# Performance work log

Hardware: AMD Instinct MI355X
Metric: run time of the kernel (lower is better)

Reference implementation:

```python
import jax, jax.numpy as jnp
import numpy as np

HID = 3584   # hidden_size
NH = 28      # num_attention_heads
NKV = 4      # num_key_value_heads
HD = 128     # head_dim
S = 4        # packed samples
L = 1024     # tokens per sample (sample_lens = [L]*S)
T = S * L
THETA = 1000000.0
EPS = 1e-6


def rmsnorm(x, w):
    # Qwen2NavitRMSNorm (fp32 math)
    v = jnp.mean(x * x, axis=-1, keepdims=True)
    return w * (x * jax.lax.rsqrt(v + EPS))


def rotate_half(x):
    d = x.shape[-1] // 2
    return jnp.concatenate([-x[..., d:], x[..., :d]], axis=-1)


def setup_inputs() -> dict:
    key = jax.random.key(0)
    ks = jax.random.split(key, 12)
    sc = 0.02
    x = jax.random.normal(ks[0], (T, HID), jnp.float32)
    # rotary embeddings: positions restart per packed sample
    pos = jnp.tile(jnp.arange(L, dtype=jnp.float32), S)
    inv = 1.0 / (THETA ** (jnp.arange(0, HD, 2, dtype=jnp.float32) / HD))
    fr = pos[:, None] * inv[None, :]
    emb = jnp.concatenate([fr, fr], axis=-1)  # [T, HD]
    und_idx = jnp.arange(0, T, 2, dtype=jnp.int32)  # interleaved und/gen tokens
    gen_idx = jnp.arange(1, T, 2, dtype=jnp.int32)
    n = lambda k, shp: jax.random.normal(k, shp, jnp.float32) * sc
    return dict(
        packed_sequence=x, cos=jnp.cos(emb), sin=jnp.sin(emb),
        wq=n(ks[1], (NH * HD, HID)), bq=jnp.zeros((NH * HD,), jnp.float32),
        wk=n(ks[2], (NKV * HD, HID)), bk=jnp.zeros((NKV * HD,), jnp.float32),
        wv=n(ks[3], (NKV * HD, HID)), bv=jnp.zeros((NKV * HD,), jnp.float32),
        wo=n(ks[4], (HID, NH * HD)),
        wqg=n(ks[5], (NH * HD, HID)), bqg=jnp.zeros((NH * HD,), jnp.float32),
        wkg=n(ks[6], (NKV * HD, HID)), bkg=jnp.zeros((NKV * HD,), jnp.float32),
        wvg=n(ks[7], (NKV * HD, HID)), bvg=jnp.zeros((NKV * HD,), jnp.float32),
        wog=n(ks[8], (HID, NH * HD)),
        qn=jnp.ones((HD,), jnp.float32), kn=jnp.ones((HD,), jnp.float32),
        qng=jnp.ones((HD,), jnp.float32), kng=jnp.ones((HD,), jnp.float32),
        und_idx=und_idx, gen_idx=gen_idx,
    )


def reference(packed_sequence, cos, sin, wq, bq, wk, bk, wv, bv, wo,
              wqg, bqg, wkg, bkg, wvg, bvg, wog, qn, kn, qng, kng,
              und_idx, gen_idx):
    x = packed_sequence
    xu = x[und_idx]
    xg = x[gen_idx]

    def dual_proj(wu, bu, wg, bg, dim):
        out = jnp.zeros((T, dim), x.dtype)
        out = out.at[und_idx].set(xu @ wu.T + bu)
        out = out.at[gen_idx].set(xg @ wg.T + bg)
        return out

    q = dual_proj(wq, bq, wqg, bqg, NH * HD).reshape(T, NH, HD)
    k = dual_proj(wk, bk, wkg, bkg, NKV * HD).reshape(T, NKV, HD)
    v = dual_proj(wv, bv, wvg, bvg, NKV * HD).reshape(T, NKV, HD)

    # per-modality qk RMSNorm
    q = jnp.zeros_like(q).at[und_idx].set(rmsnorm(q[und_idx], qn)).at[gen_idx].set(rmsnorm(q[gen_idx], qng))
    k = jnp.zeros_like(k).at[und_idx].set(rmsnorm(k[und_idx], kn)).at[gen_idx].set(rmsnorm(k[gen_idx], kng))

    # RoPE (unsqueeze_dim=1 -> broadcast over heads)
    c = cos[:, None, :]
    s = sin[:, None, :]
    q = q * c + rotate_half(q) * s
    k = k * c + rotate_half(k) * s

    # GQA expand kv heads (consecutive repeat matches repeat+reshape in torch)
    grp = NH // NKV
    k = jnp.repeat(k, grp, axis=1)  # [T, NH, HD]
    v = jnp.repeat(v, grp, axis=1)

    # packed -> per-sample causal attention (all sample_lens equal)
    qh = q.reshape(S, L, NH, HD)
    kh = k.reshape(S, L, NH, HD)
    vh = v.reshape(S, L, NH, HD)
    scores = jnp.einsum('slhd,smhd->shlm', qh, kh) / np.float32(np.sqrt(HD))
    causal = jnp.tril(jnp.ones((L, L), bool))
    scores = jnp.where(causal, scores, jnp.float32(-1e30))
    p = jax.nn.softmax(scores, axis=-1)
    attn = jnp.einsum('shlm,smhd->slhd', p, vh).reshape(T, NH * HD)

    out = jnp.zeros((T, HID), x.dtype)
    out = out.at[und_idx].set(attn[und_idx] @ wo.T)
    out = out.at[gen_idx].set(attn[gen_idx] @ wog.T)
    return out
```

## Files before the change

### kernel.cpp

```cpp
#include <hip/hip_runtime.h>
#include <hip/hip_bf16.h>

#define T_TOK 4096
#define HID   3584
#define NH    28
#define NKV   4
#define HD    128
#define SEG   4
#define LSEQ  1024
#define KDIM  3584
#define BKG   64
#define NCVT  128

typedef __attribute__((ext_vector_type(8))) short bf16x8;
typedef __attribute__((ext_vector_type(4))) float f32x4;

#define GLOAD16(g, l) __builtin_amdgcn_global_load_lds( \
    (const __attribute__((address_space(1))) void*)(g), \
    (__attribute__((address_space(3))) void*)(l), 16, 0, 0)

__device__ __forceinline__ unsigned short f2bf(float f) {
    unsigned u = __float_as_uint(f);
    return (unsigned short)((u + 0x7fffu + ((u >> 16) & 1u)) >> 16);
}
__device__ __forceinline__ float bf2f(unsigned short u) {
    return __uint_as_float(((unsigned)u) << 16);
}

__device__ __forceinline__ f32x4 mfma16(bf16x8 a, bf16x8 b, f32x4 c) {
    return __builtin_amdgcn_mfma_f32_16x16x32_bf16(a, b, c, 0, 0, 0);
}

#define XN4  3670016
#define WQ4  3211264
#define WK4  458752
__global__ void cvt_front(const float* __restrict__ x,
                          const float* __restrict__ wq, const float* __restrict__ wqg,
                          const float* __restrict__ wk, const float* __restrict__ wkg,
                          const float* __restrict__ wv, const float* __restrict__ wvg,
                          unsigned short* __restrict__ xu, unsigned short* __restrict__ xg,
                          unsigned short* __restrict__ wqb, unsigned short* __restrict__ wqgb,
                          unsigned short* __restrict__ wkb, unsigned short* __restrict__ wkgb,
                          unsigned short* __restrict__ wvb, unsigned short* __restrict__ wvgb) {
    size_t i = (size_t)blockIdx.x * 256 + threadIdx.x;
    if (i < XN4) {
        int t = (int)(i / (HID / 4));
        int c = (int)(i - (size_t)t * (HID / 4));
        float4 v = reinterpret_cast<const float4*>(x)[i];
        ushort4 o;
        o.x = f2bf(v.x); o.y = f2bf(v.y); o.z = f2bf(v.z); o.w = f2bf(v.w);
        unsigned short* dst = ((t & 1) ? xg : xu) + (size_t)(t >> 1) * HID + c * 4;
        *reinterpret_cast<ushort4*>(dst) = o;
        return;
    }
    i -= XN4;
    const float* s; unsigned short* d;
    if (i < 2 * (size_t)WQ4) {
        if (i < WQ4) { s = wq; d = wqb; } else { i -= WQ4; s = wqg; d = wqgb; }
    } else {
        i -= 2 * (size_t)WQ4;
        size_t seg = i / WK4; i -= seg * WK4;
        switch (seg) {
            case 0: s = wk;  d = wkb;  break;
            case 1: s = wkg; d = wkgb; break;
            case 2: s = wv;  d = wvb;  break;
            default: s = wvg; d = wvgb; break;
        }
    }
    float4 v = reinterpret_cast<const float4*>(s)[i];
    ushort4 o;
    o.x = f2bf(v.x); o.y = f2bf(v.y); o.z = f2bf(v.z); o.w = f2bf(v.w);
    reinterpret_cast<ushort4*>(d)[i] = o;
}

__device__ __forceinline__ void gemm256_core(const unsigned short* __restrict__ Aptr,
                                             const unsigned short* __restrict__ Bptr,
                                             unsigned short* ldsbase, f32x4 (&acc)[8][4],
                                             int kb, int kend) {
    const int tid = threadIdx.x;
    const int lane = tid & 63, w = tid >> 6;
    const int wr = w >> 2, wc = w & 3;
    const int lr = lane & 15, lkg = lane >> 4;
    char* const L = (char*)ldsbase;

    int src_off[4];
#pragma unroll
    for (int j = 0; j < 4; j++) {
        int r = j * 64 + (tid >> 3);
        int clog = (tid & 7) ^ ((tid >> 3) & 7);
        src_off[j] = r * KDIM + clog * 8;
    }
    const int aoff0 = (wr * 128 + lr) * 128 + ((lkg ^ (lr & 7)) << 4);
    const int boff0 = (wc * 64 + lr) * 128 + ((lkg ^ (lr & 7)) << 4) + 32768;

    bf16x8 a[4][2], b[4][2];
#pragma unroll
    for (int m = 0; m < 8; m++)
#pragma unroll
        for (int n = 0; n < 4; n++) acc[m][n] = (f32x4){0.f, 0.f, 0.f, 0.f};

#define STG_A(buf, k0, h) do { _Pragma("unroll") for (int jj = 0; jj < 2; jj++) { \
    int j = (h) * 2 + jj; \
    GLOAD16(Aptr + src_off[j] + (k0), L + (buf) * 65536 + j * 8192 + tid * 16); } } while (0)
#define STG_B(buf, k0, h) do { _Pragma("unroll") for (int jj = 0; jj < 2; jj++) { \
    int j = (h) * 2 + jj; \
    GLOAD16(Bptr + src_off[j] + (k0), L + (buf) * 65536 + 32768 + j * 8192 + tid * 16); } } while (0)
#define RD_A(buf, mh) do { _Pragma("unroll") for (int mm = 0; mm < 4; mm++) { \
    int ro = (buf) * 65536 + aoff0 + ((mh) * 4 + mm) * 2048; \
    a[mm][0] = *(const bf16x8*)(L + ro); \
    a[mm][1] = *(const bf16x8*)(L + (ro ^ 64)); } } while (0)
#define RD_B(buf, nh) do { _Pragma("unroll") for (int nn = 0; nn < 2; nn++) { \
    int ro = (buf) * 65536 + boff0 + ((nh) * 2 + nn) * 2048; \
    b[(nh) * 2 + nn][0] = *(const bf16x8*)(L + ro); \
    b[(nh) * 2 + nn][1] = *(const bf16x8*)(L + (ro ^ 64)); } } while (0)
#define MM(mh, nh) do { _Pragma("unroll") for (int mm = 0; mm < 4; mm++) \
    _Pragma("unroll") for (int nn = 0; nn < 2; nn++) \
    _Pragma("unroll") for (int ks = 0; ks < 2; ks++) \
        acc[(mh) * 4 + mm][(nh) * 2 + nn] = \
            mfma16(a[mm][ks], b[(nh) * 2 + nn][ks], acc[(mh) * 4 + mm][(nh) * 2 + nn]); } while (0)
#define BAR   asm volatile("s_barrier" ::: "memory")
#define LGKM0 do { asm volatile("s_waitcnt lgkmcnt(0)" ::: "memory"); \
                   __builtin_amdgcn_sched_barrier(0); } while (0)
#define VMC4  asm volatile("s_waitcnt vmcnt(4)" ::: "memory")
#define PHI   __builtin_amdgcn_s_setprio(1)
#define PLO   __builtin_amdgcn_s_setprio(0)

    STG_A(0, kb, 0); STG_A(0, kb, 1); STG_B(0, kb, 0); STG_B(0, kb, 1);
    STG_B(1, kb + BKG, 0); STG_B(1, kb + BKG, 1);
    VMC4;
    BAR;

    const int iters = (kend - kb) / (2 * BKG);
#pragma unroll 1
    for (int t = 0; t < iters; ++t) {
        int k1 = kb + (2 * t + 1) * BKG;
        int k2 = kb + (2 * t + 2) * BKG; if (k2 > kend - BKG) k2 = kend - BKG;
        int k3 = kb + (2 * t + 3) * BKG; if (k3 > kend - BKG) k3 = kend - BKG;
        RD_A(0, 0); RD_B(0, 0); STG_A(1, k1, 0);
        BAR; LGKM0; PHI; MM(0, 0); PLO; BAR;
        RD_B(0, 1); STG_A(1, k1, 1);
        BAR; LGKM0; PHI; MM(0, 1); PLO; BAR;
        RD_A(0, 1); STG_B(0, k2, 0);
        BAR; LGKM0; PHI; MM(1, 0); PLO; BAR;
        STG_B(0, k2, 1);
        BAR; LGKM0; PHI; MM(1, 1); PLO; VMC4; BAR;
        RD_A(1, 0); RD_B(1, 0); STG_A(0, k2, 0);
        BAR; LGKM0; PHI; MM(0, 0); PLO; BAR;
        RD_B(1, 1); STG_A(0, k2, 1);
        BAR; LGKM0; PHI; MM(0, 1); PLO; BAR;
        RD_A(1, 1); STG_B(1, k3, 0);
        BAR; LGKM0; PHI; MM(1, 0); PLO; BAR;
        STG_B(1, k3, 1);
        BAR; LGKM0; PHI; MM(1, 1); PLO; VMC4; BAR;
    }
    asm volatile("s_waitcnt vmcnt(0)" ::: "memory");

#undef STG_A
#undef STG_B
#undef RD_A
#undef RD_B
#undef MM
#undef BAR
#undef LGKM0
#undef VMC4
#undef PHI
#undef PLO
}

__global__ __launch_bounds__(512, 2) void qkv_gemm8(
    const unsigned short* __restrict__ xu, const unsigned short* __restrict__ xg,
    const unsigned short* __restrict__ wq0, const unsigned short* __restrict__ wk0,
    const unsigned short* __restrict__ wv0, const unsigned short* __restrict__ wq1,
    const unsigned short* __restrict__ wk1, const unsigned short* __restrict__ wv1,
    const float* __restrict__ bq0, const float* __restrict__ bk0, const float* __restrict__ bv0,
    const float* __restrict__ bq1, const float* __restrict__ bk1, const float* __restrict__ bv1,
    unsigned short* __restrict__ qp, unsigned short* __restrict__ kp,
    unsigned short* __restrict__ vp) {
    __shared__ unsigned short lds[65536];
    const int bid = blockIdx.x;
    int nb, ks, bm, kb, klen;
    if (bid < 256) {
        int g = bid >> 6;
        int rem = bid & 63;
        ks = rem >> 4; bm = rem & 15;
        nb = 14 + g;
        kb = ks * 896; klen = 896;
    } else {
        int e = bid - 256;
        nb = e >> 4; bm = e & 15;
        ks = 0; kb = 0; klen = KDIM;
    }
    const int par = bm >> 3, mb = bm & 7;
    const unsigned short* A = (par ? xg : xu) + (size_t)mb * 256 * KDIM;
    const unsigned short* W;
    const float* bias;
    unsigned short* C;
    int ldc, col0;
    if (nb < 14) {
        W = (par ? wq1 : wq0) + (size_t)nb * 256 * KDIM;
        bias = (par ? bq1 : bq0); C = qp; ldc = NH * HD; col0 = nb * 256;
    } else if (nb < 16) {
        W = (par ? wk1 : wk0) + (size_t)(nb - 14) * 256 * KDIM;
        bias = (par ? bk1 : bk0); C = kp + (size_t)ks * T_TOK * (NKV * HD);
        ldc = NKV * HD; col0 = (nb - 14) * 256;
    } else {
        W = (par ? wv1 : wv0) + (size_t)(nb - 16) * 256 * KDIM;
        bias = (par ? bv1 : bv0); C = vp + (size_t)ks * T_TOK * (NKV * HD);
        ldc = NKV * HD; col0 = (nb - 16) * 256;
    }
    f32x4 acc[8][4];
    gemm256_core(A, W, lds, acc, kb, kb + klen);

    const int lane = threadIdx.x & 63, w = threadIdx.x >> 6;
    const int wr = w >> 2, wc = w & 3, lr = lane & 15, lkg = lane >> 4;
#pragma unroll
    for (int n = 0; n < 4; n++) {
        int colt = col0 + wc * 64 + n * 16 + lr;
        float bb = (ks == 0) ? bias[colt] : 0.f;
#pragma unroll
        for (int m = 0; m < 8; m++) {
#pragma unroll
            for (int rg = 0; rg < 4; rg++) {
                int tr = mb * 256 + wr * 128 + m * 16 + lkg * 4 + rg;
                int tok = 2 * tr + par;
                C[(size_t)tok * ldc + colt] = f2bf(acc[m][n][rg] + bb);
            }
        }
    }
}

__global__ __launch_bounds__(512, 2) void oproj_gemm8(
    const unsigned short* __restrict__ au, const unsigned short* __restrict__ ag,
    const unsigned short* __restrict__ wo0, const unsigned short* __restrict__ wo1,
    float* __restrict__ out) {
    __shared__ unsigned short lds[65536];
    const int bid = blockIdx.x;
    const int x = bid & 7, i = bid >> 3;
    const int nb = i >> 1, bm = x * 2 + (i & 1);
    const int par = bm >> 3, mb = bm & 7;
    const unsigned short* A = (par ? ag : au) + (size_t)mb * 256 * KDIM;
    const unsigned short* W = (par ? wo1 : wo0) + (size_t)nb * 256 * KDIM;
    f32x4 acc[8][4];
    gemm256_core(A, W, lds, acc, 0, KDIM);

    const int lane = threadIdx.x & 63, w = threadIdx.x >> 6;
    const int wr = w >> 2, wc = w & 3, lr = lane & 15, lkg = lane >> 4;
#pragma unroll
    for (int n = 0; n < 4; n++) {
        int col = nb * 256 + wc * 64 + n * 16 + lr;
#pragma unroll
        for (int m = 0; m < 8; m++) {
#pragma unroll
            for (int rg = 0; rg < 4; rg++) {
                int tr = mb * 256 + wr * 128 + m * 16 + lkg * 4 + rg;
                int tok = 2 * tr + par;
                out[(size_t)tok * HID + col] = acc[m][n][rg];
            }
        }
    }
}

__global__ void normrope2(const unsigned short* __restrict__ qp, const unsigned short* __restrict__ kp,
                          const unsigned short* __restrict__ vp,
                          const float* __restrict__ cosb, const float* __restrict__ sinb,
                          const float* __restrict__ qn, const float* __restrict__ kn,
                          const float* __restrict__ qng, const float* __restrict__ kng,
                          unsigned short* __restrict__ q_bf, unsigned short* __restrict__ k_bf,
                          unsigned short* __restrict__ vT) {
    if (blockIdx.y == 8) {
        if (blockIdx.x >= 1024) return;
        const int u = blockIdx.x * 2 + (threadIdx.x >> 7);
        const int d = threadIdx.x & 127;
        const int sh = u >> 7, lb = u & 127;
        const int s = sh >> 2, hv = sh & 3;
        const size_t S = (size_t)T_TOK * NKV * HD;
        unsigned short tmp[8];
#pragma unroll
        for (int i = 0; i < 8; i++) {
            size_t idx = ((size_t)(s * LSEQ + lb * 8 + i)) * (NKV * HD) + hv * HD + d;
            tmp[i] = f2bf(bf2f(vp[idx]) + bf2f(vp[S + idx]) +
                          bf2f(vp[2 * S + idx]) + bf2f(vp[3 * S + idx]));
        }
        *(bf16x8*)(vT + ((size_t)sh * HD + d) * LSEQ + lb * 8) = *(bf16x8*)tmp;
        return;
    }
    const int t = blockIdx.x, w = threadIdx.x >> 6, lane = threadIdx.x & 63;
    const int h = blockIdx.y * 4 + w;
    const bool isq = (h < 28);
    float v0, v1;
    if (isq) {
        const unsigned short* src = qp + (size_t)t * (NH * HD) + h * HD;
        v0 = bf2f(src[lane]);
        v1 = bf2f(src[lane + 64]);
    } else {
        const unsigned short* src = kp + (size_t)t * (NKV * HD) + (h - 28) * HD;
        const size_t S = (size_t)T_TOK * NKV * HD;
        v0 = bf2f(src[lane]) + bf2f(src[S + lane]) + bf2f(src[2 * S + lane]) + bf2f(src[3 * S + lane]);
        v1 = bf2f(src[lane + 64]) + bf2f(src[S + lane + 64]) +
             bf2f(src[2 * S + lane + 64]) + bf2f(src[3 * S + lane + 64]);
    }
    float ss = v0 * v0 + v1 * v1;
#pragma unroll
    for (int off = 32; off >= 1; off >>= 1) ss += __shfl_xor(ss, off, 64);
    float inv = rsqrtf(ss * (1.f / 128.f) + 1e-6f);
    const float* wn = isq ? ((t & 1) ? qng : qn) : ((t & 1) ? kng : kn);
    float n0 = v0 * inv * wn[lane], n1 = v1 * inv * wn[lane + 64];
    float c0 = cosb[(size_t)t * HD + lane], c1 = cosb[(size_t)t * HD + lane + 64];
    float s0 = sinb[(size_t)t * HD + lane], s1 = sinb[(size_t)t * HD + lane + 64];
    float o0 = n0 * c0 - n1 * s0;
    float o1 = n1 * c1 + n0 * s1;
    unsigned short* dst = isq ? q_bf + (size_t)t * (NH * HD) + h * HD
                              : k_bf + (size_t)t * (NKV * HD) + (h - 28) * HD;
    dst[lane] = f2bf(o0);
    dst[lane + 64] = f2bf(o1);
}

__global__ __launch_bounds__(512, 4) void attn_fwd(
    const unsigned short* __restrict__ q_bf, const unsigned short* __restrict__ k_bf,
    const unsigned short* __restrict__ vT,
    unsigned short* __restrict__ au, unsigned short* __restrict__ ag,
    const float* __restrict__ wof, const float* __restrict__ wogf,
    unsigned short* __restrict__ wob, unsigned short* __restrict__ wogb) {
    __shared__ unsigned short kt[2][64 * 128];
    __shared__ unsigned short vt[2][128 * 64];
    __shared__ unsigned short pt[8][16 * 64];

    const int bid = blockIdx.x;
    const int tid = threadIdx.x;
    if (bid < NCVT) {
        const size_t n4 = (size_t)KDIM * KDIM / 4;
        for (size_t i = (size_t)bid * 512 + tid; i < 2 * n4; i += (size_t)NCVT * 512) {
            const float* sp = (i < n4) ? wof : wogf;
            unsigned short* dp = (i < n4) ? wob : wogb;
            size_t j = (i < n4) ? i : i - n4;
            float4 v = reinterpret_cast<const float4*>(sp)[j];
            ushort4 o;
            o.x = f2bf(v.x); o.y = f2bf(v.y); o.z = f2bf(v.z); o.w = f2bf(v.w);
            reinterpret_cast<ushort4*>(dp)[j] = o;
        }
        return;
    }
    const int e = bid - NCVT;
    const int qbk = 7 - (e / 112);
    const int rem = e % 112;
    const int h = rem >> 2, s = rem & 3;
    const int hk = h / 7;
    const int lane = tid & 63, w = tid >> 6;
    const int lr = lane & 15, lkg = lane >> 4;
    const int qg = qbk * 128 + w * 16 + lr;

    bf16x8 qf[4];
    {
        const unsigned short* qp =
            q_bf + ((size_t)(s * LSEQ + qg)) * (NH * HD) + h * HD;
#pragma unroll
        for (int kk = 0; kk < 4; kk++) qf[kk] = *(const bf16x8*)(qp + kk * 32 + lkg * 8);
    }
    asm volatile("s_waitcnt vmcnt(0)" ::: "memory");

    float m_r = -1e30f, l_r = 0.f;
    f32x4 accO[8];
#pragma unroll
    for (int dn = 0; dn < 8; dn++) accO[dn] = (f32x4){0.f, 0.f, 0.f, 0.f};

    const float scale = 0.08838834764831843f;
    const int nkt = 2 * qbk + 2;

#define STAGE_KV(buf, ktile) do { _Pragma("unroll") for (int i = 0; i < 2; i++) { \
    int o = i * 8192 + tid * 16; \
    { int r = o >> 8; int sc = ((o >> 4) & 15) ^ (r & 7); \
      GLOAD16(k_bf + ((size_t)(s * LSEQ + (ktile) * 64 + r)) * (NKV * HD) + hk * HD + sc * 8, \
              (char*)kt[buf] + o); } \
    { int r = o >> 7; int sc = ((o >> 4) & 7) ^ (r & 7); \
      GLOAD16(vT + ((size_t)((s * NKV + hk) * HD + r)) * LSEQ + (ktile) * 64 + sc * 8, \
              (char*)vt[buf] + o); } } } while (0)

    STAGE_KV(0, 0);

#pragma unroll 1
    for (int ktile = 0; ktile < nkt; ++ktile) {
        const int cur = ktile & 1;
        if (ktile + 1 < nkt) {
            STAGE_KV(cur ^ 1, ktile + 1);
            asm volatile("s_waitcnt vmcnt(4)" ::: "memory");
        } else {
            asm volatile("s_waitcnt vmcnt(0)" ::: "memory");
        }
        asm volatile("s_barrier" ::: "memory");

        f32x4 accT[4];
#pragma unroll
        for (int n = 0; n < 4; n++) accT[n] = (f32x4){0.f, 0.f, 0.f, 0.f};
#pragma unroll
        for (int n = 0; n < 4; n++) {
            int r = n * 16 + lr;
#pragma unroll
            for (int kk = 0; kk < 4; kk++) {
                bf16x8 kf = *(const bf16x8*)((const char*)kt[cur] + r * 256 +
                                             (((kk * 4 + lkg) ^ (r & 7)) << 4));
                accT[n] = mfma16(kf, qf[kk], accT[n]);
            }
        }
        float mnew = -1e30f;
#pragma unroll
        for (int n = 0; n < 4; n++) {
#pragma unroll
            for (int rg = 0; rg < 4; rg++) {
                int kvg = ktile * 64 + n * 16 + lkg * 4 + rg;
                float sv = accT[n][rg] * scale;
                sv = (kvg <= qg) ? sv : -1e30f;
                accT[n][rg] = sv;
                mnew = fmaxf(mnew, sv);
            }
        }
        mnew = fmaxf(mnew, __shfl_xor(mnew, 16, 64));
        mnew = fmaxf(mnew, __shfl_xor(mnew, 32, 64));
        if (__any(mnew > m_r + 8.f)) {
            float mc = fmaxf(m_r, mnew);
            float alpha = __expf(m_r - mc);
            m_r = mc;
            l_r *= alpha;
            float ab[4];
#pragma unroll
            for (int rg = 0; rg < 4; rg++) ab[rg] = __shfl(alpha, lkg * 4 + rg, 64);
#pragma unroll
            for (int dn = 0; dn < 8; dn++)
#pragma unroll
                for (int rg = 0; rg < 4; rg++) accO[dn][rg] *= ab[rg];
        }
        float ls = 0.f;
#pragma unroll
        for (int n = 0; n < 4; n++) {
            unsigned short p4[4];
#pragma unroll
            for (int rg = 0; rg < 4; rg++) {
                float p = __expf(accT[n][rg] - m_r);
                ls += p;
                p4[rg] = f2bf(p);
            }
            int byte = lr * 128 + ((((n * 2 + (lkg >> 1)) ^ (lr & 7))) << 4) + (lkg & 1) * 8;
            *(uint2*)((char*)pt[w] + byte) = *(uint2*)p4;
        }
        ls += __shfl_xor(ls, 16, 64);
        ls += __shfl_xor(ls, 32, 64);
        l_r += ls;
#pragma unroll
        for (int kk2 = 0; kk2 < 2; kk2++) {
            bf16x8 pf = *(const bf16x8*)((const char*)pt[w] + lr * 128 +
                                         (((kk2 * 4 + lkg) ^ (lr & 7)) << 4));
#pragma unroll
            for (int dn = 0; dn < 8; dn++) {
                int r2 = dn * 16 + lr;
                bf16x8 vf = *(const bf16x8*)((const char*)vt[cur] + r2 * 128 +
                                             (((kk2 * 4 + lkg) ^ (r2 & 7)) << 4));
                accO[dn] = mfma16(pf, vf, accO[dn]);
            }
        }
        asm volatile("s_barrier" ::: "memory");
    }
#undef STAGE_KV

    float lb4[4];
#pragma unroll
    for (int rg = 0; rg < 4; rg++) lb4[rg] = __shfl(l_r, lkg * 4 + rg, 64);
#pragma unroll
    for (int dn = 0; dn < 8; dn++) {
#pragma unroll
        for (int rg = 0; rg < 4; rg++) {
            int row = qbk * 128 + w * 16 + lkg * 4 + rg;
            int t = s * LSEQ + row;
            unsigned short* dst = ((t & 1) ? ag : au) + (size_t)(t >> 1) * (NH * HD) +
                                  h * HD + dn * 16 + lr;
            *dst = f2bf(accO[dn][rg] / lb4[rg]);
        }
    }
}

extern "C" void kernel_launch(void* const* d_in, const int* in_sizes, int n_in,
                              void* d_out, int out_size, void* d_ws, size_t ws_size,
                              hipStream_t stream) {
    const float* x    = (const float*)d_in[0];
    const float* cosb = (const float*)d_in[1];
    const float* sinb = (const float*)d_in[2];
    const float* wq   = (const float*)d_in[3];
    const float* bq   = (const float*)d_in[4];
    const float* wk   = (const float*)d_in[5];
    const float* bk   = (const float*)d_in[6];
    const float* wv   = (const float*)d_in[7];
    const float* bv   = (const float*)d_in[8];
    const float* wo   = (const float*)d_in[9];
    const float* wqg  = (const float*)d_in[10];
    const float* bqg  = (const float*)d_in[11];
    const float* wkg  = (const float*)d_in[12];
    const float* bkg  = (const float*)d_in[13];
    const float* wvg  = (const float*)d_in[14];
    const float* bvg  = (const float*)d_in[15];
    const float* wog  = (const float*)d_in[16];
    const float* qn   = (const float*)d_in[17];
    const float* kn   = (const float*)d_in[18];
    const float* qng  = (const float*)d_in[19];
    const float* kng  = (const float*)d_in[20];
    float* out = (float*)d_out;

    char* ws = (char*)d_ws;
    size_t off = 0;
    auto alloc = [&](size_t bytes) -> char* {
        char* p = ws + off;
        off += (bytes + 255) & ~(size_t)255;
        return p;
    };
    const size_t WQ_E = (size_t)3584 * 3584;
    const size_t WK_E = (size_t)512 * 3584;
    unsigned short* wqb  = (unsigned short*)alloc(WQ_E * 2);
    unsigned short* wqgb = (unsigned short*)alloc(WQ_E * 2);
    unsigned short* wob  = (unsigned short*)alloc(WQ_E * 2);
    unsigned short* wogb = (unsigned short*)alloc(WQ_E * 2);
    unsigned short* wkb  = (unsigned short*)alloc(WK_E * 2);
    unsigned short* wkgb = (unsigned short*)alloc(WK_E * 2);
    unsigned short* wvb  = (unsigned short*)alloc(WK_E * 2);
    unsigned short* wvgb = (unsigned short*)alloc(WK_E * 2);
    unsigned short* xu   = (unsigned short*)alloc((size_t)2048 * HID * 2);
    unsigned short* xg   = (unsigned short*)alloc((size_t)2048 * HID * 2);
    unsigned short* qp = (unsigned short*)alloc((size_t)T_TOK * (NH * HD) * 2);
    unsigned short* kp = (unsigned short*)alloc((size_t)4 * T_TOK * (NKV * HD) * 2);
    unsigned short* vp = (unsigned short*)alloc((size_t)4 * T_TOK * (NKV * HD) * 2);
    unsigned short* q_bf = wqb;
    unsigned short* k_bf = wqb + (size_t)T_TOK * (NH * HD);
    unsigned short* vTb  = k_bf + (size_t)T_TOK * (NKV * HD);
    unsigned short* au = qp;
    unsigned short* ag = au + (size_t)2048 * (NH * HD);

    if (ws_size < off) return;

    cvt_front<<<dim3((XN4 + 2 * WQ4 + 4 * WK4) / 256), 256, 0, stream>>>(
        x, wq, wqg, wk, wkg, wv, wvg,
        xu, xg, wqb, wqgb, wkb, wkgb, wvb, wvgb);

    qkv_gemm8<<<dim3(480), 512, 0, stream>>>(xu, xg, wqb, wkb, wvb, wqgb, wkgb, wvgb,
                                             bq, bk, bv, bqg, bkg, bvg, qp, kp, vp);
    normrope2<<<dim3(T_TOK, 9), 256, 0, stream>>>(qp, kp, vp, cosb, sinb,
                                                  qn, kn, qng, kng, q_bf, k_bf, vTb);
    attn_fwd<<<dim3(NCVT + 896), 512, 0, stream>>>(q_bf, k_bf, vTb, au, ag,
                                                   wo, wog, wob, wogb);
    oproj_gemm8<<<dim3(224), 512, 0, stream>>>(au, ag, wob, wogb, out);
}
```

Before: 394.0 us.

## Read K/V fragments directly from global memory and shrink attention blocks to 64 queries

The attention kernel no longer stages K and V tiles into LDS with async double-buffered loads and barriers. Each wave now loads its MFMA operands straight from global memory. Blocks shrink from 512 to 256 threads (64 query rows), so twice as many blocks are launched. This removes LDS staging and block-wide barriers but relies on L2/cache for K/V reuse across waves, adding redundant global traffic and exposing load latency without software pipelining.

```diff
diff --git a/kernel.cpp b/kernel.cpp
--- a/kernel.cpp
+++ b/kernel.cpp
@@ -315,21 +315,19 @@
     dst[lane + 64] = f2bf(o1);
 }
 
-__global__ __launch_bounds__(512, 4) void attn_fwd(
+__global__ __launch_bounds__(256, 4) void attn_fwd(
     const unsigned short* __restrict__ q_bf, const unsigned short* __restrict__ k_bf,
     const unsigned short* __restrict__ vT,
     unsigned short* __restrict__ au, unsigned short* __restrict__ ag,
     const float* __restrict__ wof, const float* __restrict__ wogf,
     unsigned short* __restrict__ wob, unsigned short* __restrict__ wogb) {
-    __shared__ unsigned short kt[2][64 * 128];
-    __shared__ unsigned short vt[2][128 * 64];
-    __shared__ unsigned short pt[8][16 * 64];
+    __shared__ unsigned short pt[4][16 * 64];
 
     const int bid = blockIdx.x;
     const int tid = threadIdx.x;
     if (bid < NCVT) {
         const size_t n4 = (size_t)KDIM * KDIM / 4;
-        for (size_t i = (size_t)bid * 512 + tid; i < 2 * n4; i += (size_t)NCVT * 512) {
+        for (size_t i = (size_t)bid * 256 + tid; i < 2 * n4; i += (size_t)NCVT * 256) {
             const float* sp = (i < n4) ? wof : wogf;
             unsigned short* dp = (i < n4) ? wob : wogb;
             size_t j = (i < n4) ? i : i - n4;
@@ -341,13 +339,13 @@
         return;
     }
     const int e = bid - NCVT;
-    const int qbk = 7 - (e / 112);
+    const int qbk = 15 - (e / 112);
     const int rem = e % 112;
     const int h = rem >> 2, s = rem & 3;
     const int hk = h / 7;
     const int lane = tid & 63, w = tid >> 6;
     const int lr = lane & 15, lkg = lane >> 4;
-    const int qg = qbk * 128 + w * 16 + lr;
+    const int qg = qbk * 64 + w * 16 + lr;
 
     bf16x8 qf[4];
     {
@@ -356,7 +354,6 @@
 #pragma unroll
         for (int kk = 0; kk < 4; kk++) qf[kk] = *(const bf16x8*)(qp + kk * 32 + lkg * 8);
     }
-    asm volatile("s_waitcnt vmcnt(0)" ::: "memory");
 
     float m_r = -1e30f, l_r = 0.f;
     f32x4 accO[8];
@@ -364,40 +361,20 @@
     for (int dn = 0; dn < 8; dn++) accO[dn] = (f32x4){0.f, 0.f, 0.f, 0.f};
 
     const float scale = 0.08838834764831843f;
-    const int nkt = 2 * qbk + 2;
-
-#define STAGE_KV(buf, ktile) do { _Pragma("unroll") for (int i = 0; i < 2; i++) { \
-    int o = i * 8192 + tid * 16; \
-    { int r = o >> 8; int sc = ((o >> 4) & 15) ^ (r & 7); \
-      GLOAD16(k_bf + ((size_t)(s * LSEQ + (ktile) * 64 + r)) * (NKV * HD) + hk * HD + sc * 8, \
-              (char*)kt[buf] + o); } \
-    { int r = o >> 7; int sc = ((o >> 4) & 7) ^ (r & 7); \
-      GLOAD16(vT + ((size_t)((s * NKV + hk) * HD + r)) * LSEQ + (ktile) * 64 + sc * 8, \
-              (char*)vt[buf] + o); } } } while (0)
-
-    STAGE_KV(0, 0);
+    const int nkt = qbk + 1;
 
 #pragma unroll 1
     for (int ktile = 0; ktile < nkt; ++ktile) {
-        const int cur = ktile & 1;
-        if (ktile + 1 < nkt) {
-            STAGE_KV(cur ^ 1, ktile + 1);
-            asm volatile("s_waitcnt vmcnt(4)" ::: "memory");
-        } else {
-            asm volatile("s_waitcnt vmcnt(0)" ::: "memory");
-        }
-        asm volatile("s_barrier" ::: "memory");
-
+        const unsigned short* kbase =
+            k_bf + ((size_t)(s * LSEQ + ktile * 64 + lr)) * (NKV * HD) + hk * HD + lkg * 8;
         f32x4 accT[4];
 #pragma unroll
         for (int n = 0; n < 4; n++) accT[n] = (f32x4){0.f, 0.f, 0.f, 0.f};
 #pragma unroll
         for (int n = 0; n < 4; n++) {
-            int r = n * 16 + lr;
 #pragma unroll
             for (int kk = 0; kk < 4; kk++) {
-                bf16x8 kf = *(const bf16x8*)((const char*)kt[cur] + r * 256 +
-                                             (((kk * 4 + lkg) ^ (r & 7)) << 4));
+                bf16x8 kf = *(const bf16x8*)(kbase + n * 16 * (NKV * HD) + kk * 32);
                 accT[n] = mfma16(kf, qf[kk], accT[n]);
             }
         }
@@ -444,21 +421,19 @@
         ls += __shfl_xor(ls, 16, 64);
         ls += __shfl_xor(ls, 32, 64);
         l_r += ls;
+        const unsigned short* vbase =
+            vT + ((size_t)((s * NKV + hk) * HD + lr)) * LSEQ + ktile * 64 + lkg * 8;
 #pragma unroll
         for (int kk2 = 0; kk2 < 2; kk2++) {
             bf16x8 pf = *(const bf16x8*)((const char*)pt[w] + lr * 128 +
                                          (((kk2 * 4 + lkg) ^ (lr & 7)) << 4));
 #pragma unroll
             for (int dn = 0; dn < 8; dn++) {
-                int r2 = dn * 16 + lr;
-                bf16x8 vf = *(const bf16x8*)((const char*)vt[cur] + r2 * 128 +
-                                             (((kk2 * 4 + lkg) ^ (r2 & 7)) << 4));
+                bf16x8 vf = *(const bf16x8*)(vbase + dn * 16 * LSEQ + kk2 * 32);
                 accO[dn] = mfma16(pf, vf, accO[dn]);
             }
         }
-        asm volatile("s_barrier" ::: "memory");
-    }
-#undef STAGE_KV
+    }
 
     float lb4[4];
 #pragma unroll
@@ -467,7 +442,7 @@
     for (int dn = 0; dn < 8; dn++) {
 #pragma unroll
         for (int rg = 0; rg < 4; rg++) {
-            int row = qbk * 128 + w * 16 + lkg * 4 + rg;
+            int row = qbk * 64 + w * 16 + lkg * 4 + rg;
             int t = s * LSEQ + row;
             unsigned short* dst = ((t & 1) ? ag : au) + (size_t)(t >> 1) * (NH * HD) +
                                   h * HD + dn * 16 + lr;
@@ -540,7 +515,7 @@
                                              bq, bk, bv, bqg, bkg, bvg, qp, kp, vp);
     normrope2<<<dim3(T_TOK, 9), 256, 0, stream>>>(qp, kp, vp, cosb, sinb,
                                                   qn, kn, qng, kng, q_bf, k_bf, vTb);
-    attn_fwd<<<dim3(NCVT + 896), 512, 0, stream>>>(q_bf, k_bf, vTb, au, ag,
-                                                   wo, wog, wob, wogb);
+    attn_fwd<<<dim3(NCVT + 1792), 256, 0, stream>>>(q_bf, k_bf, vTb, au, ag,
+                                                    wo, wog, wob, wogb);
     oproj_gemm8<<<dim3(224), 512, 0, stream>>>(au, ag, wob, wogb, out);
 }
```

Result: slower. 547.9 us (+39.1%).
